# Optimization experiments

Measured on AMD Instinct MI355X. Metric: run time of the kernel, lower is better.

## Reference

```python
import jax, jax.numpy as jnp
import numpy as np

MARGIN = 0.5          # triplet_margin
CLS_W = 1.0           # classification_weight
TRI_W = 1.0           # triplet_weight
SMOOTH = 0.1          # CrossEntropyLoss label_smoothing
PD_EPS = 1e-6         # torch pairwise_distance eps inside TripletMarginLoss


def setup_inputs() -> dict:
    key = jax.random.key(0)
    k1, k2, k3 = jax.random.split(key, 3)
    B, D, C = 8192, 128, 1000
    logits = jax.random.normal(k1, (B, C), dtype=jnp.float32)
    emb = jax.random.normal(k2, (B, D), dtype=jnp.float32)
    emb = emb / jnp.linalg.norm(emb, axis=1, keepdims=True)  # L2-normalized per docstring
    labels = jax.random.randint(k3, (B,), 0, C, dtype=jnp.int32)
    return {"logits": logits, "embeddings": emb, "labels": labels}


def _combined_loss(logits, embeddings, labels):
    # --- cross entropy with label smoothing 0.1 ---
    logp = jax.nn.log_softmax(logits, axis=-1)
    nll = -jnp.take_along_axis(logp, labels[:, None], axis=-1)[:, 0]
    smooth_term = -logp.mean(axis=-1)  # eps/C * sum(-logp) == eps * mean(-logp)
    cls_loss = ((1.0 - SMOOTH) * nll + SMOOTH * smooth_term).mean()

    # --- batch-hard triplet mining (vectorized over all rows) ---
    B = embeddings.shape[0]
    sq = jnp.sum(embeddings * embeddings, axis=1)
    # squared pairwise distances [B,B]; monotone in true distance, so ranking matches cdist
    d2 = sq[:, None] + sq[None, :] - 2.0 * (embeddings @ embeddings.T)
    eq = labels[:, None] == labels[None, :]
    pos_mask = eq & ~jnp.eye(B, dtype=bool)   # same class, not self
    neg_mask = ~eq
    big = jnp.finfo(d2.dtype).max
    hardest_pos = jnp.argmax(jnp.where(pos_mask, d2, -big), axis=1)  # farthest positive
    hardest_neg = jnp.argmin(jnp.where(neg_mask, d2, big), axis=1)   # closest negative
    valid = pos_mask.any(axis=1) & neg_mask.any(axis=1)

    # --- TripletMarginLoss(margin, p=2) over valid triplets ---
    a = embeddings
    p = embeddings[hardest_pos]
    n = embeddings[hardest_neg]
    d_ap = jnp.linalg.norm(a - p + PD_EPS, axis=1)  # torch adds eps inside the norm
    d_an = jnp.linalg.norm(a - n + PD_EPS, axis=1)
    per_row = jnp.maximum(d_ap - d_an + MARGIN, 0.0)
    cnt = jnp.sum(valid)
    triplet_loss = jnp.where(
        cnt > 0,
        jnp.sum(jnp.where(valid, per_row, 0.0)) / jnp.maximum(cnt, 1).astype(per_row.dtype),
        jnp.zeros((), per_row.dtype),
    )

    return CLS_W * cls_loss + TRI_W * triplet_loss


def reference(logits, embeddings, labels):
    return _combined_loss(logits, embeddings, labels)
```

## Files before the change

### kernel.cpp

```cpp
#include <hip/hip_runtime.h>

#define NB 8192
#define ND 128
#define NC 1000
#define NJC 16
#define JCB 4
#define JBS 128
#define NIS 32
#define CAP 64
#define NRB (NB / 4)

typedef __attribute__((ext_vector_type(8))) short bf16x8;
typedef __attribute__((ext_vector_type(4))) float f32x4;

__device__ __forceinline__ unsigned short f2bf(float f) {
    unsigned int u = __float_as_uint(f);
    return (unsigned short)((u + 0x7fffu + ((u >> 16) & 1u)) >> 16);
}

__global__ __launch_bounds__(256) void ce_prep_kernel(const float* __restrict__ logits,
                                                      const float* __restrict__ emb,
                                                      const int* __restrict__ labels,
                                                      unsigned short* __restrict__ ebf,
                                                      float* __restrict__ cls_part,
                                                      int* __restrict__ cnt) {
    int wave = threadIdx.x >> 6, lane = threadIdx.x & 63;
    int r = blockIdx.x * 4 + wave;

    if (blockIdx.x == 0) {
        for (int k = threadIdx.x; k < NC; k += 256) cnt[k] = 0;
    }

    {
        const float* erow = emb + (size_t)r * ND;
        float2 v = *(const float2*)(erow + lane * 2);
        unsigned int packed = (unsigned int)f2bf(v.x) | ((unsigned int)f2bf(v.y) << 16);
        *(unsigned int*)(ebf + (size_t)r * ND + lane * 2) = packed;
    }

    const float* x = logits + (size_t)r * NC;
    float4 q0 = *(const float4*)(x + 4 * lane);
    float4 q1 = *(const float4*)(x + 256 + 4 * lane);
    float4 q2 = *(const float4*)(x + 512 + 4 * lane);
    float4 q3;
    bool a3 = (192 + lane) < 250;
    if (a3) q3 = *(const float4*)(x + 768 + 4 * lane);
    else q3 = make_float4(-3.4e38f, -3.4e38f, -3.4e38f, -3.4e38f);

    float m = fmaxf(fmaxf(fmaxf(q0.x, q0.y), fmaxf(q0.z, q0.w)),
                    fmaxf(fmaxf(q1.x, q1.y), fmaxf(q1.z, q1.w)));
    m = fmaxf(m, fmaxf(fmaxf(q2.x, q2.y), fmaxf(q2.z, q2.w)));
    m = fmaxf(m, fmaxf(fmaxf(q3.x, q3.y), fmaxf(q3.z, q3.w)));
    float s = (q0.x + q0.y + q0.z + q0.w) + (q1.x + q1.y + q1.z + q1.w) +
              (q2.x + q2.y + q2.z + q2.w) +
              (a3 ? (q3.x + q3.y + q3.z + q3.w) : 0.f);
#pragma unroll
    for (int o = 32; o >= 1; o >>= 1) {
        m = fmaxf(m, __shfl_xor(m, o));
        s += __shfl_xor(s, o);
    }
    float se = expf(q0.x - m) + expf(q0.y - m) + expf(q0.z - m) + expf(q0.w - m) +
               expf(q1.x - m) + expf(q1.y - m) + expf(q1.z - m) + expf(q1.w - m) +
               expf(q2.x - m) + expf(q2.y - m) + expf(q2.z - m) + expf(q2.w - m) +
               expf(q3.x - m) + expf(q3.y - m) + expf(q3.z - m) + expf(q3.w - m);
#pragma unroll
    for (int o = 32; o >= 1; o >>= 1) se += __shfl_xor(se, o);
    float xl = x[labels[r]];
    float v = (m + logf(se)) - 0.9f * xl - 0.1f * (s * (1.0f / NC));
    if (lane == 0) cls_part[r] = v;
}

__global__ __launch_bounds__(256) void bucket_kernel(const int* __restrict__ labels,
                                                     int* __restrict__ cnt,
                                                     int* __restrict__ lists) {
    int r = blockIdx.x * 256 + threadIdx.x;
    int c = labels[r];
    int slot = atomicAdd(&cnt[c], 1);
    if (slot < CAP) lists[c * CAP + slot] = r;
}

__global__ __launch_bounds__(512, 2) void mine_kernel(const unsigned short* __restrict__ ebf,
                                                      const int* __restrict__ labels,
                                                      float* __restrict__ part) {
    __shared__ unsigned short btile[2][JBS * ND];
    __shared__ int pj_lb[JCB * JBS];
    int tid = threadIdx.x;
    int wave = tid >> 6, lane = tid & 63;
    int col = lane & 15, grp = lane >> 4;
    int jchunk = blockIdx.x, jcbase = jchunk * (JCB * JBS);
    int ibase = blockIdx.y * 256 + wave * 32;

#define STAGE(buf, jb0)                                                                 \
    do {                                                                                \
        _Pragma("unroll")                                                               \
        for (int rep = 0; rep < 4; ++rep) {                                             \
            int row = (tid >> 4) + rep * 32;                                            \
            const unsigned short* src =                                                 \
                ebf + (size_t)((jb0) + row) * ND + (((tid & 15) ^ (row & 7)) << 3);     \
            unsigned short* dst =                                                       \
                &btile[buf][0] + (size_t)((tid >> 6) * 4 + rep * 32) * ND;              \
            __builtin_amdgcn_global_load_lds(                                           \
                (const __attribute__((address_space(1))) unsigned int*)src,             \
                (__attribute__((address_space(3))) unsigned int*)dst, 16, 0, 0);        \
        }                                                                               \
    } while (0)

    STAGE(0, jcbase);
    pj_lb[tid] = labels[jcbase + tid];

    bf16x8 af[2][4];
#pragma unroll
    for (int ic = 0; ic < 2; ++ic) {
        const unsigned short* ap = ebf + (size_t)(ibase + ic * 16 + col) * ND + (grp << 3);
#pragma unroll
        for (int kc = 0; kc < 4; ++kc) af[ic][kc] = *(const bf16x8*)(ap + kc * 32);
    }
    int li[8];
#pragma unroll
    for (int ic = 0; ic < 2; ++ic)
#pragma unroll
        for (int r = 0; r < 4; ++r) li[ic * 4 + r] = labels[ibase + ic * 16 + grp * 4 + r];

    float bn[8];
#pragma unroll
    for (int k = 0; k < 8; ++k) bn[k] = -3.4e38f;

    __syncthreads();

#pragma unroll
    for (int t = 0; t < JCB; ++t) {
        if (t + 1 < JCB) STAGE((t + 1) & 1, jcbase + (t + 1) * JBS);

        const unsigned short* bt = &btile[t & 1][0];
#pragma unroll
        for (int st = 0; st < 8; ++st) {
            bf16x8 bfr[4];
#pragma unroll
            for (int kc = 0; kc < 4; ++kc) {
                int chunk = (grp + 4 * kc) ^ (col & 7);
                bfr[kc] = *(const bf16x8*)(bt + (size_t)(st * 16 + col) * ND + chunk * 8);
            }
            f32x4 acc[2] = {{0.f, 0.f, 0.f, 0.f}, {0.f, 0.f, 0.f, 0.f}};
#pragma unroll
            for (int kc = 0; kc < 4; ++kc)
#pragma unroll
                for (int ic = 0; ic < 2; ++ic)
                    acc[ic] = __builtin_amdgcn_mfma_f32_16x16x32_bf16(af[ic][kc], bfr[kc],
                                                                      acc[ic], 0, 0, 0);
            int lj = pj_lb[t * JBS + st * 16 + col];
#pragma unroll
            for (int ic = 0; ic < 2; ++ic)
#pragma unroll
                for (int r = 0; r < 4; ++r)
                    bn[ic * 4 + r] =
                        fmaxf(bn[ic * 4 + r], (lj == li[ic * 4 + r]) ? -3.4e38f : acc[ic][r]);
        }

        if (t + 1 < JCB) __syncthreads();
    }
#undef STAGE

#pragma unroll
    for (int k = 0; k < 8; ++k)
#pragma unroll
        for (int msk = 1; msk <= 8; msk <<= 1)
            bn[k] = fmaxf(bn[k], __shfl_xor(bn[k], msk));
    if (col == 0) {
#pragma unroll
        for (int ic = 0; ic < 2; ++ic)
#pragma unroll
            for (int r = 0; r < 4; ++r) {
                int gi = ibase + ic * 16 + grp * 4 + r;
                part[((size_t)gi << 4) + jchunk] = bn[ic * 4 + r];
            }
    }
}

__global__ __launch_bounds__(256) void reduce_kernel(const float* __restrict__ e,
                                                     const int* __restrict__ labels,
                                                     const float* __restrict__ part,
                                                     const int* __restrict__ cnt,
                                                     const int* __restrict__ lists,
                                                     const float* __restrict__ cls_part,
                                                     float4* __restrict__ blk) {
    __shared__ float sp[4], sv[4], sc[4];
    int wave = threadIdx.x >> 6, lane = threadIdx.x & 63;
    int r = blockIdx.x * 4 + wave;
    int g = lane >> 3, sl = lane & 7;

    float nb = part[((size_t)r << 4) + (lane & 15)];
#pragma unroll
    for (int o = 1; o <= 8; o <<= 1) nb = fmaxf(nb, __shfl_xor(nb, o));
    float d_an = sqrtf(fmaxf(2.0f - 2.0f * nb, 0.0f));

    int myl = labels[r];
    int ctot = cnt[myl];
    int n = min(ctot, CAP);
    const float* a = e + (size_t)r * ND;

    float4 a0 = *(const float4*)(a + sl * 16);
    float4 a1 = *(const float4*)(a + sl * 16 + 4);
    float4 a2 = *(const float4*)(a + sl * 16 + 8);
    float4 a3 = *(const float4*)(a + sl * 16 + 12);

    float best = -1.0f;
    int jp = r;
    for (int base = 0; base < n; base += 8) {
        int idx = base + g;
        bool ok = (idx < n);
        int j2 = ok ? lists[myl * CAP + idx] : r;
        const float* p = e + (size_t)j2 * ND;
        float4 p0 = *(const float4*)(p + sl * 16);
        float4 p1 = *(const float4*)(p + sl * 16 + 4);
        float4 p2 = *(const float4*)(p + sl * 16 + 8);
        float4 p3 = *(const float4*)(p + sl * 16 + 12);
        float d, ss = 0.f;
        d = a0.x - p0.x; ss += d * d; d = a0.y - p0.y; ss += d * d;
        d = a0.z - p0.z; ss += d * d; d = a0.w - p0.w; ss += d * d;
        d = a1.x - p1.x; ss += d * d; d = a1.y - p1.y; ss += d * d;
        d = a1.z - p1.z; ss += d * d; d = a1.w - p1.w; ss += d * d;
        d = a2.x - p2.x; ss += d * d; d = a2.y - p2.y; ss += d * d;
        d = a2.z - p2.z; ss += d * d; d = a2.w - p2.w; ss += d * d;
        d = a3.x - p3.x; ss += d * d; d = a3.y - p3.y; ss += d * d;
        d = a3.z - p3.z; ss += d * d; d = a3.w - p3.w; ss += d * d;
        ss += __shfl_xor(ss, 1);
        ss += __shfl_xor(ss, 2);
        ss += __shfl_xor(ss, 4);
        float d2v = (ok && j2 != r) ? ss : -2.0f;
        if (d2v > best || (d2v == best && j2 < jp)) { best = d2v; jp = j2; }
    }
#pragma unroll
    for (int msk = 8; msk <= 32; msk <<= 1) {
        float ob = __shfl_xor(best, msk);
        int oj = __shfl_xor(jp, msk);
        if (ob > best || (ob == best && oj < jp)) { best = ob; jp = oj; }
    }
    bool valid = (ctot >= 2) && (ctot < NB);

    const float* p = e + (size_t)jp * ND;
    float2 av = *(const float2*)(a + lane * 2);
    float2 pv = *(const float2*)(p + lane * 2);
    float dx = av.x - pv.x + 1e-6f, dy = av.y - pv.y + 1e-6f;
    float ss = dx * dx + dy * dy;
#pragma unroll
    for (int o = 32; o >= 1; o >>= 1) ss += __shfl_xor(ss, o);
    float d_ap = sqrtf(ss);

    if (lane == 0) {
        sp[wave] = valid ? fmaxf(d_ap - d_an + 0.5f, 0.0f) : 0.0f;
        sv[wave] = valid ? 1.0f : 0.0f;
        sc[wave] = cls_part[r];
    }
    __syncthreads();
    if (threadIdx.x == 0)
        blk[blockIdx.x] = make_float4(sp[0] + sp[1] + sp[2] + sp[3],
                                      sv[0] + sv[1] + sv[2] + sv[3],
                                      sc[0] + sc[1] + sc[2] + sc[3], 0.f);
}

__global__ __launch_bounds__(1024) void fin_kernel(const float4* __restrict__ blk,
                                                   float* __restrict__ out) {
    __shared__ float sc[16], sp[16], sn[16];
    int t = threadIdx.x;
    int wave = t >> 6, lane = t & 63;
    float tp = 0.f, tv = 0.f, c = 0.f;
    for (int k = t; k < NRB; k += 1024) {
        float4 q = blk[k];
        tp += q.x;
        tv += q.y;
        c += q.z;
    }
#pragma unroll
    for (int o = 32; o >= 1; o >>= 1) {
        tp += __shfl_xor(tp, o);
        tv += __shfl_xor(tv, o);
        c += __shfl_xor(c, o);
    }
    if (lane == 0) { sp[wave] = tp; sn[wave] = tv; sc[wave] = c; }
    __syncthreads();
    if (t == 0) {
        float P = 0.f, V = 0.f, C = 0.f;
        for (int w = 0; w < 16; ++w) { P += sp[w]; V += sn[w]; C += sc[w]; }
        float tri = V > 0.5f ? P / V : 0.0f;
        out[0] = C * (1.0f / NB) + tri;
    }
}

extern "C" void kernel_launch(void* const* d_in, const int* in_sizes, int n_in,
                              void* d_out, int out_size, void* d_ws, size_t ws_size,
                              hipStream_t stream) {
    const float* logits = (const float*)d_in[0];
    const float* emb = (const float*)d_in[1];
    const int* labels = (const int*)d_in[2];

    char* w = (char*)d_ws;
    unsigned short* ebf = (unsigned short*)w;
    float* part = (float*)(w + 2097152);
    float* cls_part = (float*)(w + 2621440);
    int* cnt = (int*)(w + 2654208);
    int* lists = (int*)(w + 2658304);
    float4* blk = (float4*)(w + 2920448);

    ce_prep_kernel<<<NB / 4, 256, 0, stream>>>(logits, emb, labels, ebf, cls_part, cnt);
    bucket_kernel<<<NB / 256, 256, 0, stream>>>(labels, cnt, lists);
    mine_kernel<<<dim3(NJC, NIS), 512, 0, stream>>>(ebf, labels, part);
    reduce_kernel<<<NRB, 256, 0, stream>>>(emb, labels, part, cnt, lists, cls_part, blk);
    fin_kernel<<<1, 1024, 0, stream>>>(blk, (float*)d_out);
}
```

Baseline: 53.10 us.

## Exploit Gram matrix symmetry: compute only upper-triangular tile pairs in mining

The mining kernel now launches one block per upper-triangular pair of 128-row chunks. Each block computes one 128x128 dot-product tile and writes both row maxima and column maxima, so the symmetric lower half is never computed and the MFMA work is roughly halved. The partial-max buffer grows from 16 to 64 slices per row, and the reduce kernel is widened to match. Costs include a larger workspace, a triangular index decode loop per block, an extra column reduction through shared memory, and loss of the previous double-buffered tile pipelining.

```diff
diff --git a/kernel.cpp b/kernel.cpp
--- a/kernel.cpp
+++ b/kernel.cpp
@@ -3,10 +3,9 @@
 #define NB 8192
 #define ND 128
 #define NC 1000
-#define NJC 16
-#define JCB 4
-#define JBS 128
-#define NIS 32
+#define NCH 64
+#define CHS 128
+#define NPAIR (NCH * (NCH + 1) / 2)
 #define CAP 64
 #define NRB (NB / 4)
 
@@ -79,34 +78,32 @@
     if (slot < CAP) lists[c * CAP + slot] = r;
 }
 
-__global__ __launch_bounds__(512, 2) void mine_kernel(const unsigned short* __restrict__ ebf,
+__global__ __launch_bounds__(256, 4) void mine_kernel(const unsigned short* __restrict__ ebf,
                                                       const int* __restrict__ labels,
                                                       float* __restrict__ part) {
-    __shared__ unsigned short btile[2][JBS * ND];
-    __shared__ int pj_lb[JCB * JBS];
+    __shared__ unsigned short btile[CHS * ND];
+    __shared__ float colbuf[4][CHS];
     int tid = threadIdx.x;
     int wave = tid >> 6, lane = tid & 63;
     int col = lane & 15, grp = lane >> 4;
-    int jchunk = blockIdx.x, jcbase = jchunk * (JCB * JBS);
-    int ibase = blockIdx.y * 256 + wave * 32;
-
-#define STAGE(buf, jb0)                                                                 \
-    do {                                                                                \
-        _Pragma("unroll")                                                               \
-        for (int rep = 0; rep < 4; ++rep) {                                             \
-            int row = (tid >> 4) + rep * 32;                                            \
-            const unsigned short* src =                                                 \
-                ebf + (size_t)((jb0) + row) * ND + (((tid & 15) ^ (row & 7)) << 3);     \
-            unsigned short* dst =                                                       \
-                &btile[buf][0] + (size_t)((tid >> 6) * 4 + rep * 32) * ND;              \
-            __builtin_amdgcn_global_load_lds(                                           \
-                (const __attribute__((address_space(1))) unsigned int*)src,             \
-                (__attribute__((address_space(3))) unsigned int*)dst, 16, 0, 0);        \
-        }                                                                               \
-    } while (0)
-
-    STAGE(0, jcbase);
-    pj_lb[tid] = labels[jcbase + tid];
+
+    int t = blockIdx.x, a = 0;
+    while (t >= NCH - a) { t -= NCH - a; ++a; }
+    int b = a + t;
+
+    int ibase = a * CHS + wave * 32;
+    int jbase = b * CHS;
+
+#pragma unroll
+    for (int rep = 0; rep < 8; ++rep) {
+        int row = (tid >> 4) + rep * 16;
+        const unsigned short* src =
+            ebf + (size_t)(jbase + row) * ND + (((tid & 15) ^ (row & 7)) << 3);
+        unsigned short* dst = btile + (size_t)((tid >> 6) * 4 + rep * 16) * ND;
+        __builtin_amdgcn_global_load_lds(
+            (const __attribute__((address_space(1))) unsigned int*)src,
+            (__attribute__((address_space(3))) unsigned int*)dst, 16, 0, 0);
+    }
 
     bf16x8 af[2][4];
 #pragma unroll
@@ -120,45 +117,46 @@
     for (int ic = 0; ic < 2; ++ic)
 #pragma unroll
         for (int r = 0; r < 4; ++r) li[ic * 4 + r] = labels[ibase + ic * 16 + grp * 4 + r];
+    int ljall[8];
+#pragma unroll
+    for (int st = 0; st < 8; ++st) ljall[st] = labels[jbase + st * 16 + col];
 
     float bn[8];
-#pragma unroll
-    for (int k = 0; k < 8; ++k) bn[k] = -3.4e38f;
+    float colmax[8];
+#pragma unroll
+    for (int k = 0; k < 8; ++k) { bn[k] = -3.4e38f; colmax[k] = -3.4e38f; }
 
     __syncthreads();
 
 #pragma unroll
-    for (int t = 0; t < JCB; ++t) {
-        if (t + 1 < JCB) STAGE((t + 1) & 1, jcbase + (t + 1) * JBS);
-
-        const unsigned short* bt = &btile[t & 1][0];
-#pragma unroll
-        for (int st = 0; st < 8; ++st) {
-            bf16x8 bfr[4];
-#pragma unroll
-            for (int kc = 0; kc < 4; ++kc) {
-                int chunk = (grp + 4 * kc) ^ (col & 7);
-                bfr[kc] = *(const bf16x8*)(bt + (size_t)(st * 16 + col) * ND + chunk * 8);
+    for (int st = 0; st < 8; ++st) {
+        bf16x8 bfr[4];
+#pragma unroll
+        for (int kc = 0; kc < 4; ++kc) {
+            int chunk = (grp + 4 * kc) ^ (col & 7);
+            bfr[kc] = *(const bf16x8*)(btile + (size_t)(st * 16 + col) * ND + chunk * 8);
+        }
+        f32x4 acc[2] = {{0.f, 0.f, 0.f, 0.f}, {0.f, 0.f, 0.f, 0.f}};
+#pragma unroll
+        for (int kc = 0; kc < 4; ++kc)
+#pragma unroll
+            for (int ic = 0; ic < 2; ++ic)
+                acc[ic] = __builtin_amdgcn_mfma_f32_16x16x32_bf16(af[ic][kc], bfr[kc],
+                                                                  acc[ic], 0, 0, 0);
+        int lj = ljall[st];
+        float cm = -3.4e38f;
+#pragma unroll
+        for (int ic = 0; ic < 2; ++ic)
+#pragma unroll
+            for (int r = 0; r < 4; ++r) {
+                float mv = (lj == li[ic * 4 + r]) ? -3.4e38f : acc[ic][r];
+                bn[ic * 4 + r] = fmaxf(bn[ic * 4 + r], mv);
+                cm = fmaxf(cm, mv);
             }
-            f32x4 acc[2] = {{0.f, 0.f, 0.f, 0.f}, {0.f, 0.f, 0.f, 0.f}};
-#pragma unroll
-            for (int kc = 0; kc < 4; ++kc)
-#pragma unroll
-                for (int ic = 0; ic < 2; ++ic)
-                    acc[ic] = __builtin_amdgcn_mfma_f32_16x16x32_bf16(af[ic][kc], bfr[kc],
-                                                                      acc[ic], 0, 0, 0);
-            int lj = pj_lb[t * JBS + st * 16 + col];
-#pragma unroll
-            for (int ic = 0; ic < 2; ++ic)
-#pragma unroll
-                for (int r = 0; r < 4; ++r)
-                    bn[ic * 4 + r] =
-                        fmaxf(bn[ic * 4 + r], (lj == li[ic * 4 + r]) ? -3.4e38f : acc[ic][r]);
-        }
-
-        if (t + 1 < JCB) __syncthreads();
-    }
-#undef STAGE
+        cm = fmaxf(cm, __shfl_xor(cm, 16));
+        cm = fmaxf(cm, __shfl_xor(cm, 32));
+        colmax[st] = cm;
+    }
 
 #pragma unroll
     for (int k = 0; k < 8; ++k)
@@ -171,8 +169,21 @@
 #pragma unroll
             for (int r = 0; r < 4; ++r) {
                 int gi = ibase + ic * 16 + grp * 4 + r;
-                part[((size_t)gi << 4) + jchunk] = bn[ic * 4 + r];
+                part[(size_t)gi * NCH + b] = bn[ic * 4 + r];
             }
+    }
+
+    if (a != b) {
+        if (lane < 16) {
+#pragma unroll
+            for (int st = 0; st < 8; ++st) colbuf[wave][st * 16 + lane] = colmax[st];
+        }
+        __syncthreads();
+        if (tid < CHS) {
+            float m = fmaxf(fmaxf(colbuf[0][tid], colbuf[1][tid]),
+                            fmaxf(colbuf[2][tid], colbuf[3][tid]));
+            part[(size_t)(jbase + tid) * NCH + a] = m;
+        }
     }
 }
 
@@ -188,9 +199,9 @@
     int r = blockIdx.x * 4 + wave;
     int g = lane >> 3, sl = lane & 7;
 
-    float nb = part[((size_t)r << 4) + (lane & 15)];
-#pragma unroll
-    for (int o = 1; o <= 8; o <<= 1) nb = fmaxf(nb, __shfl_xor(nb, o));
+    float nb = part[(size_t)r * NCH + lane];
+#pragma unroll
+    for (int o = 1; o <= 32; o <<= 1) nb = fmaxf(nb, __shfl_xor(nb, o));
     float d_an = sqrtf(fmaxf(2.0f - 2.0f * nb, 0.0f));
 
     int myl = labels[r];
@@ -296,14 +307,14 @@
     char* w = (char*)d_ws;
     unsigned short* ebf = (unsigned short*)w;
     float* part = (float*)(w + 2097152);
-    float* cls_part = (float*)(w + 2621440);
-    int* cnt = (int*)(w + 2654208);
-    int* lists = (int*)(w + 2658304);
-    float4* blk = (float4*)(w + 2920448);
+    float* cls_part = (float*)(w + 4194304);
+    int* cnt = (int*)(w + 4227072);
+    int* lists = (int*)(w + 4231168);
+    float4* blk = (float4*)(w + 4493312);
 
     ce_prep_kernel<<<NB / 4, 256, 0, stream>>>(logits, emb, labels, ebf, cls_part, cnt);
     bucket_kernel<<<NB / 256, 256, 0, stream>>>(labels, cnt, lists);
-    mine_kernel<<<dim3(NJC, NIS), 512, 0, stream>>>(ebf, labels, part);
+    mine_kernel<<<NPAIR, 256, 0, stream>>>(ebf, labels, part);
     reduce_kernel<<<NRB, 256, 0, stream>>>(emb, labels, part, cnt, lists, cls_part, blk);
     fin_kernel<<<1, 1024, 0, stream>>>(blk, (float*)d_out);
 }
```

Result: faster. 49.74 us (-6.3%).
